# Optimization experiments

Hardware: AMD Instinct MI355X
Metric: run time of the kernel (lower is better)

## Reference

```python
import jax, jax.numpy as jnp
import numpy as np

B, S, CIN, H, W, D = 8, 16, 128, 64, 64, 64


def setup_inputs() -> dict:
    key = jax.random.key(0)
    ks = jax.random.split(key, 16)
    def rn(i, shape, s=0.05):
        return jax.random.normal(ks[i], shape, dtype=jnp.float32) * s
    z = lambda *sh: jnp.zeros(sh, jnp.float32)
    return {
        "x": jax.random.normal(ks[0], (B, S, CIN, H, W), dtype=jnp.float32),
        "proj_w": rn(1, (D, CIN, 1, 1)),
        "bn_gamma": jnp.ones((D,), jnp.float32),
        "bn_beta": z(D),
        "clstm_w": rn(2, (4 * D, 2 * D, 3, 3)),
        "clstm_b": z(4 * D),
        "lq_wih": rn(3, (4 * D, D)), "lq_whh": rn(4, (4 * D, D)),
        "lq_bih": z(4 * D), "lq_bhh": z(4 * D),
        "lr_wih": rn(5, (4 * D, D)), "lr_whh": rn(6, (4 * D, D)),
        "lr_bih": z(4 * D), "lr_bhh": z(4 * D),
        "fcf_w": rn(7, (D, D)), "fcf_b": z(D),
        "fcF_w": rn(8, (D, D)), "fcF_b": z(D),
        "fcQ_w": rn(9, (D, D)), "fcQ_b": z(D),
        "fcR_w": rn(10, (D, D)), "fcR_b": z(D),
        "P_init": 0.1 * jnp.eye(D, dtype=jnp.float32),
        "fc_w": rn(11, (D, D)), "fc_b": z(D),
        "fco_w": rn(12, (1, D)), "fco_b": z(1),
        "fca_w": rn(13, (1, D)), "fca_b": z(1),
    }


def _fc(zv, w, b):
    return zv @ w.T + b


def _forward(x, proj_w, bn_gamma, bn_beta, clstm_w, clstm_b,
             lq_wih, lq_whh, lq_bih, lq_bhh, lr_wih, lr_whh, lr_bih, lr_bhh,
             fcf_w, fcf_b, fcF_w, fcF_b, fcQ_w, fcQ_b, fcR_w, fcR_b,
             P_init, fc_w, fc_b, fco_w, fco_b, fca_w, fca_b):
    Bv, Sv, C, Hv, Wv = x.shape
    Dv = P_init.shape[0]
    # 1x1 projection conv + BatchNorm2d (training-mode batch statistics)
    y = x.reshape(Bv * Sv, C, Hv, Wv)
    y = jax.lax.conv_general_dilated(y, proj_w, (1, 1), "VALID")
    mu = y.mean((0, 2, 3), keepdims=True)
    var = ((y - mu) ** 2).mean((0, 2, 3), keepdims=True)
    y = (y - mu) * jax.lax.rsqrt(var + 1e-5)
    y = y * bn_gamma[None, :, None, None] + bn_beta[None, :, None, None]
    xp = y.reshape(Bv, Sv, Dv, Hv, Wv)
    x0 = xp[:, 0]  # forward uses x[:, 0] as innovation target every step
    eye = jnp.eye(Dv, dtype=x.dtype)

    def convlstm(inp, h, c):
        zc = jax.lax.conv_general_dilated(jnp.concatenate([inp, h], axis=1), clstm_w, (1, 1), "SAME")
        zc = zc + clstm_b[None, :, None, None]
        i, f, o, g = jnp.split(zc, 4, axis=1)
        c2 = jax.nn.sigmoid(f) * c + jax.nn.sigmoid(i) * jnp.tanh(g)
        return jax.nn.sigmoid(o) * jnp.tanh(c2), c2

    def lstm_cell(zv, h, c, wih, whh, bih, bhh):  # pytorch gate order i,f,g,o
        g = zv @ wih.T + h @ whh.T + bih + bhh
        i, f, gg, o = jnp.split(g, 4, axis=-1)
        c2 = jax.nn.sigmoid(f) * c + jax.nn.sigmoid(i) * jnp.tanh(gg)
        return jax.nn.sigmoid(o) * jnp.tanh(c2), c2

    def step(carry, xs):
        y_hat, hf, cf, hQ, cQ, hR, cR, P = carry
        hf, cf = convlstm(y_hat, hf, cf)            # [B,D,H,W]
        lf = jnp.transpose(hf, (0, 2, 3, 1))        # [B,H,W,D]
        y_tick = jnp.transpose(_fc(lf, fcf_w, fcf_b), (0, 3, 1, 2))
        Fv = _fc(hf.mean((2, 3)), fcF_w, fcF_b)     # [B,D]
        FF = Fv[:, :, None] * Fv[:, None, :]        # outer product F F^T
        hQ, cQ = lstm_cell(y_tick.mean((2, 3)), hQ, cQ, lq_wih, lq_whh, lq_bih, lq_bhh)
        Qm = jnp.exp(_fc(hQ, fcQ_w, fcQ_b))[:, :, None] * eye
        hR, cR = lstm_cell(xs.mean((2, 3)), hR, cR, lr_wih, lr_whh, lr_bih, lr_bhh)
        Rm = jnp.exp(_fc(hR, fcR_w, fcR_b))[:, :, None] * eye
        P = P * FF + Qm
        K = P @ jnp.linalg.inv(P + Rm)
        IK = eye - K
        P = IK @ P @ jnp.swapaxes(IK, 1, 2) + K @ Rm @ jnp.swapaxes(K, 1, 2)
        v = x0 - y_tick
        y_hat = y_tick + jnp.einsum("bij,bjhw->bihw", K, v)
        return (y_hat, hf, cf, hQ, cQ, hR, cR, P), y_hat

    z2 = jnp.zeros((Bv, Dv, Hv, Wv), x.dtype)
    z1 = jnp.zeros((Bv, Dv), x.dtype)
    P0 = jnp.broadcast_to(P_init, (Bv, Dv, Dv))
    carry0 = (x0, z2, z2, z1, z1, z1, z1, P0)
    _, ys = jax.lax.scan(step, carry0, jnp.transpose(xp, (1, 0, 2, 3, 4)))
    feat = jnp.transpose(ys, (1, 0, 2, 3, 4)).mean((3, 4))  # [B,S,D] adaptive avgpool
    feat = jax.nn.relu(_fc(feat, fc_w, fc_b))
    offset = _fc(feat, fco_w, fco_b)
    angle = _fc(feat, fca_w, fca_b)
    return offset, angle


def reference(x, proj_w, bn_gamma, bn_beta, clstm_w, clstm_b,
              lq_wih, lq_whh, lq_bih, lq_bhh, lr_wih, lr_whh, lr_bih, lr_bhh,
              fcf_w, fcf_b, fcF_w, fcF_b, fcQ_w, fcQ_b, fcR_w, fcR_b,
              P_init, fc_w, fc_b, fco_w, fco_b, fca_w, fca_b):
    return _forward(x, proj_w, bn_gamma, bn_beta, clstm_w, clstm_b,
                    lq_wih, lq_whh, lq_bih, lq_bhh, lr_wih, lr_whh, lr_bih, lr_bhh,
                    fcf_w, fcf_b, fcF_w, fcF_b, fcQ_w, fcQ_b, fcR_w, fcR_b,
                    P_init, fc_w, fc_b, fco_w, fco_b, fca_w, fca_b)
```

## Files before the change

kernel.cpp:

```cpp
#include <hip/hip_runtime.h>
#include <math.h>


__device__ __forceinline__ float sigf(float x){ return 1.0f/(1.0f + expf(-x)); }

#define FMA4(A, W, V0, V1, V2, V3) { (A).x += (W)*(V0); (A).y += (W)*(V1); (A).z += (W)*(V2); (A).w += (W)*(V3); }

__global__ __launch_bounds__(256) void k_w3(const float* __restrict__ cw, float* __restrict__ w3){
    int idx = blockIdx.x*256 + threadIdx.x;
    if (idx < 294912){
        int col = idx & 255;
        int rk  = idx >> 8;
        int ocg = col >> 3, j = col & 7;
        int g = j >> 1, e = j & 1;
        int oc = g*64 + ocg*2 + e;
        w3[idx] = cw[oc*1152 + rk];
    }
}

__global__ __launch_bounds__(256) void k_proj(const float* __restrict__ x, const float* __restrict__ pw,
                                              float* __restrict__ x0raw, float* __restrict__ psum,
                                              float* __restrict__ psumsq){
    __shared__ __align__(16) float smem[8192];
    const int tile = blockIdx.x;
    const int n    = blockIdx.y;
    const int tid  = threadIdx.x;
    const int pj = tid & 63, dg = tid >> 6;

    for (int r = tid; r < 8192; r += 256){
        int c = r >> 6, d = r & 63;
        smem[r] = pw[d*128 + c];
    }
    __syncthreads();

    const int p0 = tile*256 + pj*4;
    float4 acc[16];
#pragma unroll
    for (int i=0;i<16;i++) acc[i] = make_float4(0.f,0.f,0.f,0.f);

    const float* xb = x + (((size_t)n) << 19) + p0;
    for (int c = 0; c < 128; ++c){
        float4 xv = *(const float4*)(xb + ((size_t)c << 12));
        const float4* wr = (const float4*)(smem + c*64 + dg*16);
#pragma unroll
        for (int q=0;q<4;++q){
            float4 w4 = wr[q];
            FMA4(acc[q*4+0], w4.x, xv.x, xv.y, xv.z, xv.w);
            FMA4(acc[q*4+1], w4.y, xv.x, xv.y, xv.z, xv.w);
            FMA4(acc[q*4+2], w4.z, xv.x, xv.y, xv.z, xv.w);
            FMA4(acc[q*4+3], w4.w, xv.x, xv.y, xv.z, xv.w);
        }
    }

    const int t = n & 15, b = n >> 4;
    if (t == 0){
#pragma unroll
        for (int i=0;i<16;i++){
            int dd = dg*16 + i;
            *(float4*)(x0raw + (((size_t)(b*64 + dd)) << 12) + p0) = acc[i];
        }
    }
    float ls[16], lss[16];
#pragma unroll
    for (int i=0;i<16;i++){
        float4 a = acc[i];
        ls[i]  = a.x + a.y + a.z + a.w;
        lss[i] = a.x*a.x + a.y*a.y + a.z*a.z + a.w*a.w;
    }
    __syncthreads();
#pragma unroll
    for (int i=0;i<16;i++) smem[pj*65 + dg*16 + i] = ls[i];
    __syncthreads();
    if (tid < 64){
        float s = 0.f;
        for (int p=0;p<64;p++) s += smem[p*65 + tid];
        psum[((n*16 + tile) << 6) + tid] = s;
    }
    __syncthreads();
#pragma unroll
    for (int i=0;i<16;i++) smem[pj*65 + dg*16 + i] = lss[i];
    __syncthreads();
    if (tid < 64){
        float s = 0.f;
        for (int p=0;p<64;p++) s += smem[p*65 + tid];
        psumsq[((n*16 + tile) << 6) + tid] = s;
    }
}

__global__ __launch_bounds__(64) void k_bnfinal(const float* __restrict__ psum, const float* __restrict__ psumsq,
                                                const float* __restrict__ gamma, const float* __restrict__ beta,
                                                float* __restrict__ scale, float* __restrict__ shift,
                                                float* __restrict__ xmean){
    const int d = threadIdx.x;
    double gs = 0.0, gss = 0.0;
    for (int n=0;n<128;n++){
        float s = 0.f, ss = 0.f;
        for (int tl=0;tl<16;tl++){
            s  += psum  [((n*16+tl)<<6) + d];
            ss += psumsq[((n*16+tl)<<6) + d];
        }
        gs += (double)s; gss += (double)ss;
    }
    double mu  = gs  / 524288.0;
    double var = gss / 524288.0 - mu*mu;
    double sc  = (double)gamma[d] / sqrt(var + 1e-5);
    float scf = (float)sc;
    float shf = (float)((double)beta[d] - mu*sc);
    scale[d] = scf; shift[d] = shf;
    for (int n=0;n<128;n++){
        float s = 0.f;
        for (int tl=0;tl<16;tl++) s += psum[((n*16+tl)<<6) + d];
        xmean[(n<<6) + d] = (s * (1.f/4096.f)) * scf + shf;
    }
}

__global__ __launch_bounds__(256) void k_zero(float* __restrict__ z){
    size_t i = ((size_t)blockIdx.x*256 + threadIdx.x)*4;
    *(float4*)(z + i) = make_float4(0.f,0.f,0.f,0.f);
}

__global__ __launch_bounds__(256) void k_init(const float* __restrict__ scale, const float* __restrict__ shift,
                                              float* __restrict__ x0, float* __restrict__ yhat_p,
                                              const float* __restrict__ Pinit, float* __restrict__ Pg,
                                              float* __restrict__ hQ, float* __restrict__ cQ,
                                              float* __restrict__ hR, float* __restrict__ cR){
    size_t idx = (size_t)blockIdx.x*256 + threadIdx.x;
    int d = (int)((idx >> 12) & 63);
    float v = x0[idx]*scale[d] + shift[d];
    x0[idx] = v;
    int b = (int)(idx >> 18), r = (int)((idx >> 6) & 63), xx = (int)(idx & 63);
    yhat_p[(((size_t)(b*64 + d))*66 + r + 1)*72 + xx + 4] = v;
    if (idx < 512){ hQ[idx]=0.f; cQ[idx]=0.f; hR[idx]=0.f; cR[idx]=0.f; }
    if (idx < 32768) Pg[idx] = Pinit[idx & 4095];
}

__global__ __launch_bounds__(256) void k_conv(const float* __restrict__ yhat_p, const float* __restrict__ hfin_p,
                                              float* __restrict__ hfout_p, float* __restrict__ cf,
                                              const float* __restrict__ w3, const float* __restrict__ cb,
                                              const float* __restrict__ fcf_w, const float* __restrict__ fcf_b,
                                              float* __restrict__ ytick,
                                              float* __restrict__ hfpart, float* __restrict__ ytpartR){
    __shared__ __align__(16) float smem[10080];
    const int IB = 9216, HS = 4352, REDZ = 8704;
    const int row = blockIdx.x;
    const int b   = blockIdx.y;
    const int tid = threadIdx.x;
    const int pxg = tid & 7;
    const int ocg = tid >> 3;
    const int px0 = pxg*8;

    float4 acc4[16];
#pragma unroll
    for (int i=0;i<16;i++) acc4[i] = make_float4(0.f,0.f,0.f,0.f);

    for (int icc = 0; icc < 32; ++icc){
        __syncthreads();
        for (int s = tid; s < 2520; s += 256){
            if (s < 2304){
                *(float4*)(smem + s*4) = ((const float4*)w3)[(size_t)icc*2304 + s];
            } else {
                int si = s - 2304;
                int icl = si/54, rem = si - icl*54, r = rem/18, x4 = rem - r*18;
                int ic  = icc*4 + icl;
                const float* f = (ic < 64) ? yhat_p : hfin_p;
                *(float4*)(smem + IB + si*4) =
                    *(const float4*)(f + (((size_t)(b*64 + (ic & 63)))*66 + row + r)*72 + x4*4);
            }
        }
        __syncthreads();
#pragma unroll
        for (int icl=0; icl<4; ++icl){
            float v[3][10];
#pragma unroll
            for (int ky=0;ky<3;++ky){
                const float* vp = smem + IB + icl*216 + ky*72 + px0;
                v[ky][0] = vp[3];
                float4 va = *(const float4*)(vp+4);
                float4 vb = *(const float4*)(vp+8);
                v[ky][1]=va.x; v[ky][2]=va.y; v[ky][3]=va.z; v[ky][4]=va.w;
                v[ky][5]=vb.x; v[ky][6]=vb.y; v[ky][7]=vb.z; v[ky][8]=vb.w;
                v[ky][9] = vp[12];
            }
#pragma unroll
            for (int k=0;k<9;++k){
                const int ky = k/3, kx = k - ky*3;
                const float* wr = smem + (icl*9+k)*256 + ocg*8;
                float4 wa  = *(const float4*)(wr);
                float4 wb4 = *(const float4*)(wr+4);
                const float u0=v[ky][kx+0], u1=v[ky][kx+1], u2=v[ky][kx+2], u3=v[ky][kx+3];
                const float u4=v[ky][kx+4], u5=v[ky][kx+5], u6=v[ky][kx+6], u7=v[ky][kx+7];
                FMA4(acc4[0],  wa.x,  u0,u1,u2,u3);  FMA4(acc4[1],  wa.x,  u4,u5,u6,u7);
                FMA4(acc4[2],  wa.y,  u0,u1,u2,u3);  FMA4(acc4[3],  wa.y,  u4,u5,u6,u7);
                FMA4(acc4[4],  wa.z,  u0,u1,u2,u3);  FMA4(acc4[5],  wa.z,  u4,u5,u6,u7);
                FMA4(acc4[6],  wa.w,  u0,u1,u2,u3);  FMA4(acc4[7],  wa.w,  u4,u5,u6,u7);
                FMA4(acc4[8],  wb4.x, u0,u1,u2,u3);  FMA4(acc4[9],  wb4.x, u4,u5,u6,u7);
                FMA4(acc4[10], wb4.y, u0,u1,u2,u3);  FMA4(acc4[11], wb4.y, u4,u5,u6,u7);
                FMA4(acc4[12], wb4.z, u0,u1,u2,u3);  FMA4(acc4[13], wb4.z, u4,u5,u6,u7);
                FMA4(acc4[14], wb4.w, u0,u1,u2,u3);  FMA4(acc4[15], wb4.w, u4,u5,u6,u7);
            }
        }
    }
    __syncthreads();

#pragma unroll
    for (int j=0;j<4;++j){
        int s = tid + j*256;
        int dp = s >> 4, c4 = s & 15;
        *(float4*)(smem + dp*68 + c4*4) = ((const float4*)fcf_w)[s];
    }

#pragma unroll
    for (int e2=0;e2<2;++e2){
        const int d = ocg*2 + e2;
        const float biv = cb[d], bfv = cb[64+d], bov = cb[128+d], bgv = cb[192+d];
        const size_t gidx = (((size_t)(b*64 + d)) << 12) + row*64 + px0;
        const size_t pidx = (((size_t)(b*64 + d))*66 + row + 1)*72 + px0 + 4;
#pragma unroll
        for (int h2=0;h2<2;++h2){
            float4 zi = acc4[(0+e2)*2 + h2];
            float4 zf = acc4[(2+e2)*2 + h2];
            float4 zo = acc4[(4+e2)*2 + h2];
            float4 zg = acc4[(6+e2)*2 + h2];
            float4 c_old = *(const float4*)(cf + gidx + h2*4);
            float4 c2, hh;
            c2.x = sigf(zf.x+bfv)*c_old.x + sigf(zi.x+biv)*tanhf(zg.x+bgv); hh.x = sigf(zo.x+bov)*tanhf(c2.x);
            c2.y = sigf(zf.y+bfv)*c_old.y + sigf(zi.y+biv)*tanhf(zg.y+bgv); hh.y = sigf(zo.y+bov)*tanhf(c2.y);
            c2.z = sigf(zf.z+bfv)*c_old.z + sigf(zi.z+biv)*tanhf(zg.z+bgv); hh.z = sigf(zo.z+bov)*tanhf(c2.z);
            c2.w = sigf(zf.w+bfv)*c_old.w + sigf(zi.w+biv)*tanhf(zg.w+bgv); hh.w = sigf(zo.w+bov)*tanhf(c2.w);
            *(float4*)(cf + gidx + h2*4) = c2;
            *(float4*)(hfout_p + pidx + h2*4) = hh;
            *(float4*)(smem + HS + d*68 + px0 + h2*4) = hh;
        }
    }
    __syncthreads();

    const int d0 = ocg*2;
    float4 yt[4];
    {
        float b0 = fcf_b[d0], b1 = fcf_b[d0+1];
        yt[0] = make_float4(b0,b0,b0,b0); yt[1] = yt[0];
        yt[2] = make_float4(b1,b1,b1,b1); yt[3] = yt[2];
    }
    for (int d=0; d<64; ++d){
        float4 h0 = *(const float4*)(smem + HS + d*68 + px0);
        float4 h1 = *(const float4*)(smem + HS + d*68 + px0 + 4);
        float w0 = smem[(d0  )*68 + d];
        float w1 = smem[(d0+1)*68 + d];
        FMA4(yt[0], w0, h0.x,h0.y,h0.z,h0.w);
        FMA4(yt[1], w0, h1.x,h1.y,h1.z,h1.w);
        FMA4(yt[2], w1, h0.x,h0.y,h0.z,h0.w);
        FMA4(yt[3], w1, h1.x,h1.y,h1.z,h1.w);
    }
#pragma unroll
    for (int e2=0;e2<2;++e2){
        const int dp = d0 + e2;
        size_t yi = (((size_t)(b*64 + dp)) << 12) + row*64 + px0;
        *(float4*)(ytick + yi)     = yt[e2*2+0];
        *(float4*)(ytick + yi + 4) = yt[e2*2+1];
        float4 a = yt[e2*2], c = yt[e2*2+1];
        smem[REDZ + dp*9 + pxg] = a.x+a.y+a.z+a.w + c.x+c.y+c.z+c.w;
    }
    __syncthreads();
    if (tid < 64){
        float s = 0.f;
#pragma unroll 8
        for (int px=0;px<64;++px) s += smem[HS + tid*68 + px];
        hfpart[((b*64 + row) << 6) + tid] = s;
        float s2 = 0.f;
#pragma unroll
        for (int q=0;q<8;++q) s2 += smem[REDZ + tid*9 + q];
        ytpartR[((b*64 + row) << 6) + tid] = s2;
    }
}

__global__ __launch_bounds__(256) void k_small(int t,
        const float* __restrict__ hfpart, const float* __restrict__ ytpartR, const float* __restrict__ xmean,
        const float* __restrict__ fcF_w, const float* __restrict__ fcF_b,
        const float* __restrict__ lq_wih, const float* __restrict__ lq_whh,
        const float* __restrict__ lq_bih, const float* __restrict__ lq_bhh,
        const float* __restrict__ lr_wih, const float* __restrict__ lr_whh,
        const float* __restrict__ lr_bih, const float* __restrict__ lr_bhh,
        const float* __restrict__ fcQ_w, const float* __restrict__ fcQ_b,
        const float* __restrict__ fcR_w, const float* __restrict__ fcR_b,
        float* __restrict__ hQ, float* __restrict__ cQ, float* __restrict__ hR, float* __restrict__ cR,
        float* __restrict__ Pg, float* __restrict__ Kg){
    const int b = blockIdx.x, tid = threadIdx.x;
    __shared__ __align__(16) float aug[64*132];
    __shared__ __align__(16) float Pl[4096];
    __shared__ float hfm[64], ytm[64], xm[64], Fv[64], Qd[64], Rd[64], rds[64];
    __shared__ float hq_s[64], cq_s[64], hr_s[64], cr_s[64];
    __shared__ float gq[256], gr[256];

    if (tid < 64){
        float s = 0.f;
        for (int r=0;r<64;r++) s += hfpart[((b*64 + r) << 6) + tid];
        hfm[tid] = s * (1.f/4096.f);
        float s2 = 0.f;
        for (int r=0;r<64;r++) s2 += ytpartR[((b*64 + r) << 6) + tid];
        ytm[tid] = s2 * (1.f/4096.f);
        xm[tid] = xmean[((b*16 + t) << 6) + tid];
        hq_s[tid] = hQ[b*64+tid]; cq_s[tid] = cQ[b*64+tid];
        hr_s[tid] = hR[b*64+tid]; cr_s[tid] = cR[b*64+tid];
    }
    __syncthreads();
    {
        int j = tid;
        float aq = lq_bih[j] + lq_bhh[j];
        float ar = lr_bih[j] + lr_bhh[j];
        for (int e=0;e<64;e++){
            aq += lq_wih[j*64+e]*ytm[e] + lq_whh[j*64+e]*hq_s[e];
            ar += lr_wih[j*64+e]*xm[e]  + lr_whh[j*64+e]*hr_s[e];
        }
        gq[j] = aq; gr[j] = ar;
    }
    if (tid < 64){
        float a = fcF_b[tid];
        for (int e=0;e<64;e++) a += fcF_w[tid*64+e]*hfm[e];
        Fv[tid] = a;
    }
    __syncthreads();
    if (tid < 64){
        int dd = tid;
        float gi = gq[dd], gf = gq[64+dd], gg = gq[128+dd], go = gq[192+dd];
        float c2 = sigf(gf)*cq_s[dd] + sigf(gi)*tanhf(gg);
        float h2 = sigf(go)*tanhf(c2);
        cq_s[dd] = c2; hq_s[dd] = h2;
        gi = gr[dd]; gf = gr[64+dd]; gg = gr[128+dd]; go = gr[192+dd];
        c2 = sigf(gf)*cr_s[dd] + sigf(gi)*tanhf(gg);
        h2 = sigf(go)*tanhf(c2);
        cr_s[dd] = c2; hr_s[dd] = h2;
    }
    __syncthreads();
    if (tid < 64){
        float aq_ = fcQ_b[tid], ar_ = fcR_b[tid];
        for (int e=0;e<64;e++){ aq_ += fcQ_w[tid*64+e]*hq_s[e]; ar_ += fcR_w[tid*64+e]*hr_s[e]; }
        Qd[tid] = expf(aq_); Rd[tid] = expf(ar_);
        hQ[b*64+tid] = hq_s[tid]; cQ[b*64+tid] = cq_s[tid];
        hR[b*64+tid] = hr_s[tid]; cR[b*64+tid] = cr_s[tid];
    }
    __syncthreads();
    for (int r = tid; r < 4096; r += 256){
        int i = r >> 6, j = r & 63;
        float p = Pg[((size_t)b << 12) + r] * Fv[i]*Fv[j] + (i==j ? Qd[i] : 0.f);
        Pl[r] = p;
        aug[i*132 + 64 + j] = p;
        aug[i*132 + j]      = p + (i==j ? Rd[i] : 0.f);
    }
    __syncthreads();
    const int r_ = tid & 63, cq_ = tid >> 6;
    for (int k = 0; k < 64; ++k){
        float akk = aug[k*132 + k];
        float f = aug[r_*132 + k] / akk;
        if (r_ != k){
#pragma unroll
            for (int u = 0; u < 8; ++u){
                int c4 = cq_*32 + u*4;
                if (c4 + 3 > k){
                    float4 pv = *(const float4*)(aug + k*132 + c4);
                    float4 av = *(const float4*)(aug + r_*132 + c4);
                    av.x = (c4+0 > k) ? av.x - f*pv.x : av.x;
                    av.y = (c4+1 > k) ? av.y - f*pv.y : av.y;
                    av.z = (c4+2 > k) ? av.z - f*pv.z : av.z;
                    av.w = (c4+3 > k) ? av.w - f*pv.w : av.w;
                    *(float4*)(aug + r_*132 + c4) = av;
                }
            }
        }
        __syncthreads();
    }
    if (tid < 64) rds[tid] = 1.0f / aug[tid*132 + tid];
    __syncthreads();
    {
        const int i = tid >> 2, jq = tid & 3;
        float4 tv[4];
#pragma unroll
        for (int q=0;q<4;++q) tv[q] = *(const float4*)(Pl + i*64 + jq*16 + q*4);
        for (int m=0;m<64;++m){
            float kim = aug[m*132 + 64 + i] * rds[m];
#pragma unroll
            for (int q=0;q<4;++q){
                float4 pv = *(const float4*)(Pl + m*64 + jq*16 + q*4);
                tv[q].x -= kim*pv.x; tv[q].y -= kim*pv.y; tv[q].z -= kim*pv.z; tv[q].w -= kim*pv.w;
            }
        }
#pragma unroll
        for (int q=0;q<4;++q) *(float4*)(aug + i*132 + jq*16 + q*4) = tv[q];
    }
    __syncthreads();
    {
        const int i = tid >> 2, jq = tid & 3;
        float4 a2[4];
#pragma unroll
        for (int q=0;q<4;++q) a2[q] = *(const float4*)(aug + i*132 + jq*16 + q*4);
        for (int m=0;m<64;++m){
            float t1im = aug[i*132 + m];
            float kim  = aug[m*132 + 64 + i] * rds[m];
            float coef = rds[m] * (kim * Rd[m] - t1im);
#pragma unroll
            for (int q=0;q<4;++q){
                float4 yv = *(const float4*)(aug + m*132 + 64 + jq*16 + q*4);
                a2[q].x += coef*yv.x; a2[q].y += coef*yv.y; a2[q].z += coef*yv.z; a2[q].w += coef*yv.w;
            }
        }
        size_t base = ((size_t)b << 12) + (size_t)i*64;
#pragma unroll
        for (int q=0;q<4;++q) *(float4*)(Pg + base + jq*16 + q*4) = a2[q];
#pragma unroll
        for (int q=0;q<4;++q){
#pragma unroll
            for (int e=0;e<4;++e){
                int j = jq*16 + q*4 + e;
                Kg[base + j] = aug[j*132 + 64 + i] * rds[j];
            }
        }
    }
}

__global__ __launch_bounds__(256) void k_apply(int t, const float* __restrict__ ytick,
                                               const float* __restrict__ x0, const float* __restrict__ Kg,
                                               float* __restrict__ yhat_p, float* __restrict__ featpart){
    __shared__ __align__(16) float kt[4160];
    const int tile = blockIdx.x;
    const int b    = blockIdx.y;
    const int tid  = threadIdx.x;
    const int pj = tid & 31, dgp = tid >> 5;

    for (int r = tid; r < 4096; r += 256){
        int i = r >> 6, j = r & 63;
        kt[j*65 + i] = Kg[((size_t)b << 12) + r];
    }
    __syncthreads();

    const int p0 = tile*128 + pj*4;
    const int rr = p0 >> 6, xx = p0 & 63;
    float4 acc[8];
#pragma unroll
    for (int i=0;i<8;i++) acc[i] = make_float4(0.f,0.f,0.f,0.f);

    for (int j = 0; j < 64; ++j){
        size_t gi = (((size_t)(b*64 + j)) << 12) + p0;
        float4 xv = *(const float4*)(x0 + gi);
        float4 yv = *(const float4*)(ytick + gi);
        float u0 = xv.x - yv.x, u1 = xv.y - yv.y, u2 = xv.z - yv.z, u3 = xv.w - yv.w;
        const float* kr = kt + j*65 + dgp*8;
#pragma unroll
        for (int il=0; il<8; ++il){
            float kv = kr[il];
            FMA4(acc[il], kv, u0,u1,u2,u3);
        }
    }
    float ls[8];
#pragma unroll
    for (int il=0;il<8;++il){
        int d = dgp*8 + il;
        size_t gi = (((size_t)(b*64 + d)) << 12) + p0;
        float4 yv = *(const float4*)(ytick + gi);
        float4 o;
        o.x = yv.x + acc[il].x; o.y = yv.y + acc[il].y; o.z = yv.z + acc[il].z; o.w = yv.w + acc[il].w;
        *(float4*)(yhat_p + (((size_t)(b*64 + d))*66 + rr + 1)*72 + xx + 4) = o;
        ls[il] = o.x + o.y + o.z + o.w;
    }
    __syncthreads();
#pragma unroll
    for (int il=0;il<8;++il) kt[pj*65 + dgp*8 + il] = ls[il];
    __syncthreads();
    if (tid < 64){
        float s = 0.f;
        for (int q=0;q<32;++q) s += kt[q*65 + tid];
        featpart[(((size_t)((t*8 + b)*32 + tile)) << 6) + tid] = s;
    }
}

__global__ __launch_bounds__(64) void k_head(const float* __restrict__ featpart,
                                             const float* __restrict__ fc_w, const float* __restrict__ fc_b,
                                             const float* __restrict__ fco_w, const float* __restrict__ fco_b,
                                             const float* __restrict__ fca_w, const float* __restrict__ fca_b,
                                             float* __restrict__ out){
    const int bt = blockIdx.x;
    const int b = bt >> 4, t = bt & 15;
    __shared__ float fs[64];
    const int i = threadIdx.x;
    float s = 0.f;
    for (int tile=0;tile<32;tile++) s += featpart[(((size_t)((t*8 + b)*32 + tile)) << 6) + i];
    fs[i] = s * (1.f/4096.f);
    __syncthreads();
    float a = fc_b[i];
    for (int e=0;e<64;e++) a += fc_w[i*64+e]*fs[e];
    a = fmaxf(a, 0.f);
    float po = a * fco_w[i];
    float pa = a * fca_w[i];
    for (int off=32; off; off >>= 1){ po += __shfl_down(po, off); pa += __shfl_down(pa, off); }
    if (i == 0){
        out[bt]       = po + fco_b[0];
        out[128 + bt] = pa + fca_b[0];
    }
}

extern "C" void kernel_launch(void* const* d_in, const int* in_sizes, int n_in,
                              void* d_out, int out_size, void* d_ws, size_t ws_size,
                              hipStream_t stream){
    const float* x       = (const float*)d_in[0];
    const float* proj_w  = (const float*)d_in[1];
    const float* bn_g    = (const float*)d_in[2];
    const float* bn_b    = (const float*)d_in[3];
    const float* clstm_w = (const float*)d_in[4];
    const float* clstm_b = (const float*)d_in[5];
    const float* lq_wih  = (const float*)d_in[6];
    const float* lq_whh  = (const float*)d_in[7];
    const float* lq_bih  = (const float*)d_in[8];
    const float* lq_bhh  = (const float*)d_in[9];
    const float* lr_wih  = (const float*)d_in[10];
    const float* lr_whh  = (const float*)d_in[11];
    const float* lr_bih  = (const float*)d_in[12];
    const float* lr_bhh  = (const float*)d_in[13];
    const float* fcf_w   = (const float*)d_in[14];
    const float* fcf_b   = (const float*)d_in[15];
    const float* fcF_w   = (const float*)d_in[16];
    const float* fcF_b   = (const float*)d_in[17];
    const float* fcQ_w   = (const float*)d_in[18];
    const float* fcQ_b   = (const float*)d_in[19];
    const float* fcR_w   = (const float*)d_in[20];
    const float* fcR_b   = (const float*)d_in[21];
    const float* P_init  = (const float*)d_in[22];
    const float* fc_w    = (const float*)d_in[23];
    const float* fc_b    = (const float*)d_in[24];
    const float* fco_w   = (const float*)d_in[25];
    const float* fco_b   = (const float*)d_in[26];
    const float* fca_w   = (const float*)d_in[27];
    const float* fca_b   = (const float*)d_in[28];
    float* out = (float*)d_out;
    float* ws  = (float*)d_ws;

    const size_t PF    = 2433024;
    const size_t FIELD = 2097152;
    float* yhat_p = ws;
    float* hfA_p  = ws + PF;
    float* hfB_p  = ws + 2*PF;
    float* cf     = ws + 3*PF;
    float* x0     = cf + FIELD;
    float* ytick  = x0 + FIELD;
    float* w3     = ytick + FIELD;
    float* psum   = w3 + 294912;
    float* psumsq = psum + 131072;
    float* scale  = psumsq + 131072;
    float* shift  = scale + 64;
    float* xmean  = shift + 64;
    float* hfpart = xmean + 8192;
    float* ytpartR= hfpart + 32768;
    float* featpart = ytpartR + 32768;
    float* hQ     = featpart + 262144;
    float* cQ     = hQ + 512;
    float* hR     = cQ + 512;
    float* cR     = hR + 512;
    float* Pg     = cR + 512;
    float* Kg     = Pg + 32768;

    hipLaunchKernelGGL(k_w3, dim3(1152), dim3(256), 0, stream, clstm_w, w3);
    hipLaunchKernelGGL(k_proj, dim3(16,128), dim3(256), 0, stream, x, proj_w, x0, psum, psumsq);
    hipLaunchKernelGGL(k_bnfinal, dim3(1), dim3(64), 0, stream, psum, psumsq, bn_g, bn_b, scale, shift, xmean);
    hipLaunchKernelGGL(k_zero, dim3(9176), dim3(256), 0, stream, ws);
    hipLaunchKernelGGL(k_init, dim3(8192), dim3(256), 0, stream, scale, shift, x0, yhat_p, P_init, Pg, hQ, cQ, hR, cR);

    for (int t = 0; t < 16; ++t){
        float* hf_in  = (t & 1) ? hfB_p : hfA_p;
        float* hf_out = (t & 1) ? hfA_p : hfB_p;
        hipLaunchKernelGGL(k_conv, dim3(64,8), dim3(256), 0, stream,
                           yhat_p, hf_in, hf_out, cf, w3, clstm_b,
                           fcf_w, fcf_b, ytick, hfpart, ytpartR);
        hipLaunchKernelGGL(k_small, dim3(8), dim3(256), 0, stream, t,
                           hfpart, ytpartR, xmean, fcF_w, fcF_b,
                           lq_wih, lq_whh, lq_bih, lq_bhh,
                           lr_wih, lr_whh, lr_bih, lr_bhh,
                           fcQ_w, fcQ_b, fcR_w, fcR_b,
                           hQ, cQ, hR, cR, Pg, Kg);
        hipLaunchKernelGGL(k_apply, dim3(32,8), dim3(256), 0, stream, t,
                           ytick, x0, Kg, yhat_p, featpart);
    }
    hipLaunchKernelGGL(k_head, dim3(128), dim3(64), 0, stream,
                       featpart, fc_w, fc_b, fco_w, fco_b, fca_w, fca_b, out);
}
```

Measured before the change: 6.465 ms.

## Restructure ConvLSTM conv to wave-uniform scalar weight loads with per-pixel threads

```diff
diff --git a/kernel.cpp b/kernel.cpp
--- a/kernel.cpp
+++ b/kernel.cpp
@@ -6,15 +6,19 @@
 
 #define FMA4(A, W, V0, V1, V2, V3) { (A).x += (W)*(V0); (A).y += (W)*(V1); (A).z += (W)*(V2); (A).w += (W)*(V3); }
 
-__global__ __launch_bounds__(256) void k_w3(const float* __restrict__ cw, float* __restrict__ w3){
+__global__ __launch_bounds__(256) void k_w4(const float* __restrict__ cw, const float* __restrict__ fcf_w,
+                                            float* __restrict__ w4, float* __restrict__ fwT){
     int idx = blockIdx.x*256 + threadIdx.x;
     if (idx < 294912){
         int col = idx & 255;
         int rk  = idx >> 8;
-        int ocg = col >> 3, j = col & 7;
-        int g = j >> 1, e = j & 1;
-        int oc = g*64 + ocg*2 + e;
-        w3[idx] = cw[oc*1152 + rk];
+        int w = col >> 5, g = (col >> 3) & 3, c = col & 7;
+        int oc = g*64 + w*8 + c;
+        w4[idx] = cw[oc*1152 + rk];
+    } else if (idx < 294912 + 4096){
+        int i = idx - 294912;
+        int ch = i >> 6, dp = i & 63;
+        fwT[i] = fcf_w[dp*64 + ch];
     }
 }
 
@@ -134,141 +138,95 @@
     if (idx < 32768) Pg[idx] = Pinit[idx & 4095];
 }
 
-__global__ __launch_bounds__(256) void k_conv(const float* __restrict__ yhat_p, const float* __restrict__ hfin_p,
+__global__ __launch_bounds__(512) void k_conv(const float* __restrict__ yhat_p, const float* __restrict__ hfin_p,
                                               float* __restrict__ hfout_p, float* __restrict__ cf,
-                                              const float* __restrict__ w3, const float* __restrict__ cb,
-                                              const float* __restrict__ fcf_w, const float* __restrict__ fcf_b,
+                                              const float* __restrict__ w4, const float* __restrict__ cb,
+                                              const float* __restrict__ fwT, const float* __restrict__ fcf_b,
                                               float* __restrict__ ytick,
                                               float* __restrict__ hfpart, float* __restrict__ ytpartR){
-    __shared__ __align__(16) float smem[10080];
-    const int IB = 9216, HS = 4352, REDZ = 8704;
+    __shared__ __align__(16) float smem[9184];
+    const int HL = 864, YL = 5024;
     const int row = blockIdx.x;
     const int b   = blockIdx.y;
     const int tid = threadIdx.x;
-    const int pxg = tid & 7;
-    const int ocg = tid >> 3;
-    const int px0 = pxg*8;
-
-    float4 acc4[16];
-#pragma unroll
-    for (int i=0;i<16;i++) acc4[i] = make_float4(0.f,0.f,0.f,0.f);
+    const int px  = tid & 63;
+    const int w   = __builtin_amdgcn_readfirstlane(tid >> 6);
+
+    float acc[4][8];
+#pragma unroll
+    for (int g=0;g<4;++g)
+#pragma unroll
+        for (int c=0;c<8;++c) acc[g][c] = 0.f;
+
+    int s_icl=0, s_r=0, s_x4=0;
+    if (tid < 216){
+        s_icl = tid/54; int rem = tid - s_icl*54; s_r = rem/18; s_x4 = rem - s_r*18;
+    }
 
     for (int icc = 0; icc < 32; ++icc){
         __syncthreads();
-        for (int s = tid; s < 2520; s += 256){
-            if (s < 2304){
-                *(float4*)(smem + s*4) = ((const float4*)w3)[(size_t)icc*2304 + s];
-            } else {
-                int si = s - 2304;
-                int icl = si/54, rem = si - icl*54, r = rem/18, x4 = rem - r*18;
-                int ic  = icc*4 + icl;
-                const float* f = (ic < 64) ? yhat_p : hfin_p;
-                *(float4*)(smem + IB + si*4) =
-                    *(const float4*)(f + (((size_t)(b*64 + (ic & 63)))*66 + row + r)*72 + x4*4);
-            }
+        if (tid < 216){
+            int ic = icc*4 + s_icl;
+            const float* f = (ic < 64) ? yhat_p : hfin_p;
+            *(float4*)(smem + tid*4) =
+                *(const float4*)(f + (((size_t)(b*64 + (ic & 63)))*66 + row + s_r)*72 + s_x4*4);
         }
         __syncthreads();
-#pragma unroll
-        for (int icl=0; icl<4; ++icl){
-            float v[3][10];
-#pragma unroll
-            for (int ky=0;ky<3;++ky){
-                const float* vp = smem + IB + icl*216 + ky*72 + px0;
-                v[ky][0] = vp[3];
-                float4 va = *(const float4*)(vp+4);
-                float4 vb = *(const float4*)(vp+8);
-                v[ky][1]=va.x; v[ky][2]=va.y; v[ky][3]=va.z; v[ky][4]=va.w;
-                v[ky][5]=vb.x; v[ky][6]=vb.y; v[ky][7]=vb.z; v[ky][8]=vb.w;
-                v[ky][9] = vp[12];
-            }
-#pragma unroll
-            for (int k=0;k<9;++k){
-                const int ky = k/3, kx = k - ky*3;
-                const float* wr = smem + (icl*9+k)*256 + ocg*8;
-                float4 wa  = *(const float4*)(wr);
-                float4 wb4 = *(const float4*)(wr+4);
-                const float u0=v[ky][kx+0], u1=v[ky][kx+1], u2=v[ky][kx+2], u3=v[ky][kx+3];
-                const float u4=v[ky][kx+4], u5=v[ky][kx+5], u6=v[ky][kx+6], u7=v[ky][kx+7];
-                FMA4(acc4[0],  wa.x,  u0,u1,u2,u3);  FMA4(acc4[1],  wa.x,  u4,u5,u6,u7);
-                FMA4(acc4[2],  wa.y,  u0,u1,u2,u3);  FMA4(acc4[3],  wa.y,  u4,u5,u6,u7);
-                FMA4(acc4[4],  wa.z,  u0,u1,u2,u3);  FMA4(acc4[5],  wa.z,  u4,u5,u6,u7);
-                FMA4(acc4[6],  wa.w,  u0,u1,u2,u3);  FMA4(acc4[7],  wa.w,  u4,u5,u6,u7);
-                FMA4(acc4[8],  wb4.x, u0,u1,u2,u3);  FMA4(acc4[9],  wb4.x, u4,u5,u6,u7);
-                FMA4(acc4[10], wb4.y, u0,u1,u2,u3);  FMA4(acc4[11], wb4.y, u4,u5,u6,u7);
-                FMA4(acc4[12], wb4.z, u0,u1,u2,u3);  FMA4(acc4[13], wb4.z, u4,u5,u6,u7);
-                FMA4(acc4[14], wb4.w, u0,u1,u2,u3);  FMA4(acc4[15], wb4.w, u4,u5,u6,u7);
-            }
-        }
-    }
-    __syncthreads();
-
-#pragma unroll
-    for (int j=0;j<4;++j){
-        int s = tid + j*256;
-        int dp = s >> 4, c4 = s & 15;
-        *(float4*)(smem + dp*68 + c4*4) = ((const float4*)fcf_w)[s];
-    }
-
-#pragma unroll
-    for (int e2=0;e2<2;++e2){
-        const int d = ocg*2 + e2;
+#pragma unroll 1
+        for (int icl = 0; icl < 4; ++icl){
+            const float* ib = smem + icl*216 + px + 3;
+            const float v0 = ib[0],   v1 = ib[1],   v2 = ib[2];
+            const float v3 = ib[72],  v4 = ib[73],  v5 = ib[74];
+            const float v6 = ib[144], v7 = ib[145], v8 = ib[146];
+            const float* wp = w4 + ((size_t)(icc*36 + icl*9) << 8) + w*32;
+#define WG(KI, VAL) { const float* q_ = wp + (KI)*256; \
+    _Pragma("unroll") for (int g=0;g<4;++g) \
+    _Pragma("unroll") for (int c=0;c<8;++c) acc[g][c] += q_[g*8+c]*(VAL); }
+            WG(0,v0) WG(1,v1) WG(2,v2)
+            WG(3,v3) WG(4,v4) WG(5,v5)
+            WG(6,v6) WG(7,v7) WG(8,v8)
+#undef WG
+        }
+    }
+
+#pragma unroll
+    for (int c=0;c<8;++c){
+        const int d = w*8 + c;
         const float biv = cb[d], bfv = cb[64+d], bov = cb[128+d], bgv = cb[192+d];
-        const size_t gidx = (((size_t)(b*64 + d)) << 12) + row*64 + px0;
-        const size_t pidx = (((size_t)(b*64 + d))*66 + row + 1)*72 + px0 + 4;
-#pragma unroll
-        for (int h2=0;h2<2;++h2){
-            float4 zi = acc4[(0+e2)*2 + h2];
-            float4 zf = acc4[(2+e2)*2 + h2];
-            float4 zo = acc4[(4+e2)*2 + h2];
-            float4 zg = acc4[(6+e2)*2 + h2];
-            float4 c_old = *(const float4*)(cf + gidx + h2*4);
-            float4 c2, hh;
-            c2.x = sigf(zf.x+bfv)*c_old.x + sigf(zi.x+biv)*tanhf(zg.x+bgv); hh.x = sigf(zo.x+bov)*tanhf(c2.x);
-            c2.y = sigf(zf.y+bfv)*c_old.y + sigf(zi.y+biv)*tanhf(zg.y+bgv); hh.y = sigf(zo.y+bov)*tanhf(c2.y);
-            c2.z = sigf(zf.z+bfv)*c_old.z + sigf(zi.z+biv)*tanhf(zg.z+bgv); hh.z = sigf(zo.z+bov)*tanhf(c2.z);
-            c2.w = sigf(zf.w+bfv)*c_old.w + sigf(zi.w+biv)*tanhf(zg.w+bgv); hh.w = sigf(zo.w+bov)*tanhf(c2.w);
-            *(float4*)(cf + gidx + h2*4) = c2;
-            *(float4*)(hfout_p + pidx + h2*4) = hh;
-            *(float4*)(smem + HS + d*68 + px0 + h2*4) = hh;
-        }
-    }
-    __syncthreads();
-
-    const int d0 = ocg*2;
-    float4 yt[4];
-    {
-        float b0 = fcf_b[d0], b1 = fcf_b[d0+1];
-        yt[0] = make_float4(b0,b0,b0,b0); yt[1] = yt[0];
-        yt[2] = make_float4(b1,b1,b1,b1); yt[3] = yt[2];
-    }
-    for (int d=0; d<64; ++d){
-        float4 h0 = *(const float4*)(smem + HS + d*68 + px0);
-        float4 h1 = *(const float4*)(smem + HS + d*68 + px0 + 4);
-        float w0 = smem[(d0  )*68 + d];
-        float w1 = smem[(d0+1)*68 + d];
-        FMA4(yt[0], w0, h0.x,h0.y,h0.z,h0.w);
-        FMA4(yt[1], w0, h1.x,h1.y,h1.z,h1.w);
-        FMA4(yt[2], w1, h0.x,h0.y,h0.z,h0.w);
-        FMA4(yt[3], w1, h1.x,h1.y,h1.z,h1.w);
-    }
-#pragma unroll
-    for (int e2=0;e2<2;++e2){
-        const int dp = d0 + e2;
-        size_t yi = (((size_t)(b*64 + dp)) << 12) + row*64 + px0;
-        *(float4*)(ytick + yi)     = yt[e2*2+0];
-        *(float4*)(ytick + yi + 4) = yt[e2*2+1];
-        float4 a = yt[e2*2], c = yt[e2*2+1];
-        smem[REDZ + dp*9 + pxg] = a.x+a.y+a.z+a.w + c.x+c.y+c.z+c.w;
-    }
-    __syncthreads();
-    if (tid < 64){
-        float s = 0.f;
+        const size_t gidx = (((size_t)(b*64 + d)) << 12) + row*64 + px;
+        float c_old = cf[gidx];
+        float c2 = sigf(acc[1][c]+bfv)*c_old + sigf(acc[0][c]+biv)*tanhf(acc[3][c]+bgv);
+        float hh = sigf(acc[2][c]+bov)*tanhf(c2);
+        cf[gidx] = c2;
+        hfout_p[(((size_t)(b*64 + d))*66 + row + 1)*72 + px + 4] = hh;
+        smem[HL + d*65 + px] = hh;
+    }
+    __syncthreads();
+
+    float yt[8];
+#pragma unroll
+    for (int j=0;j<8;++j) yt[j] = fcf_b[w*8 + j];
+    for (int ch = 0; ch < 64; ++ch){
+        float hv = smem[HL + ch*65 + px];
+        const float* fp = fwT + ch*64 + w*8;
+#pragma unroll
+        for (int j=0;j<8;++j) yt[j] += fp[j]*hv;
+    }
+#pragma unroll
+    for (int j=0;j<8;++j){
+        const int dp = w*8 + j;
+        ytick[(((size_t)(b*64 + dp)) << 12) + row*64 + px] = yt[j];
+        smem[YL + dp*65 + px] = yt[j];
+    }
+    __syncthreads();
+    if (tid < 64){
+        float s = 0.f, s2 = 0.f;
 #pragma unroll 8
-        for (int px=0;px<64;++px) s += smem[HS + tid*68 + px];
-        hfpart[((b*64 + row) << 6) + tid] = s;
-        float s2 = 0.f;
-#pragma unroll
-        for (int q=0;q<8;++q) s2 += smem[REDZ + tid*9 + q];
+        for (int pxx=0; pxx<64; ++pxx){
+            s  += smem[HL + tid*65 + pxx];
+            s2 += smem[YL + tid*65 + pxx];
+        }
+        hfpart [((b*64 + row) << 6) + tid] = s;
         ytpartR[((b*64 + row) << 6) + tid] = s2;
     }
 }
@@ -539,8 +497,9 @@
     float* cf     = ws + 3*PF;
     float* x0     = cf + FIELD;
     float* ytick  = x0 + FIELD;
-    float* w3     = ytick + FIELD;
-    float* psum   = w3 + 294912;
+    float* w4     = ytick + FIELD;
+    float* fwT    = w4 + 294912;
+    float* psum   = fwT + 4096;
     float* psumsq = psum + 131072;
     float* scale  = psumsq + 131072;
     float* shift  = scale + 64;
@@ -555,7 +514,7 @@
     float* Pg     = cR + 512;
     float* Kg     = Pg + 32768;
 
-    hipLaunchKernelGGL(k_w3, dim3(1152), dim3(256), 0, stream, clstm_w, w3);
+    hipLaunchKernelGGL(k_w4, dim3(1168), dim3(256), 0, stream, clstm_w, fcf_w, w4, fwT);
     hipLaunchKernelGGL(k_proj, dim3(16,128), dim3(256), 0, stream, x, proj_w, x0, psum, psumsq);
     hipLaunchKernelGGL(k_bnfinal, dim3(1), dim3(64), 0, stream, psum, psumsq, bn_g, bn_b, scale, shift, xmean);
     hipLaunchKernelGGL(k_zero, dim3(9176), dim3(256), 0, stream, ws);
@@ -564,9 +523,9 @@
     for (int t = 0; t < 16; ++t){
         float* hf_in  = (t & 1) ? hfB_p : hfA_p;
         float* hf_out = (t & 1) ? hfA_p : hfB_p;
-        hipLaunchKernelGGL(k_conv, dim3(64,8), dim3(256), 0, stream,
-                           yhat_p, hf_in, hf_out, cf, w3, clstm_b,
-                           fcf_w, fcf_b, ytick, hfpart, ytpartR);
+        hipLaunchKernelGGL(k_conv, dim3(64,8), dim3(512), 0, stream,
+                           yhat_p, hf_in, hf_out, cf, w4, clstm_b,
+                           fwT, fcf_b, ytick, hfpart, ytpartR);
         hipLaunchKernelGGL(k_small, dim3(8), dim3(256), 0, stream, t,
                            hfpart, ytpartR, xmean, fcF_w, fcF_b,
                            lq_wih, lq_whh, lq_bih, lq_bhh,
```

Result: faster. 5.719 ms (median of 3 runs) (-11.5%).
